# Kernel optimization log

Hardware: AMD Instinct MI355X
Metric: run time of the kernel (lower is better)

The kernel has to match this reference:

```python
import jax, jax.numpy as jnp
import numpy as np

B, T = 1024, 39
NUM_C, NUM_STU, NUM_E, EMB = 123, 100000, 50000, 256
H = 123
IN1 = NUM_C + EMB  # 379


def setup_inputs() -> dict:
    key = jax.random.key(0)
    ks = jax.random.split(key, 32)
    f = lambda k, shp, s: jax.random.normal(k, shp, dtype=jnp.float32) * s
    inp = {}
    inp["q_maritx"] = jax.random.uniform(ks[0], (B, T, NUM_C), dtype=jnp.float32)
    inp["q_maritx_next"] = jax.random.uniform(ks[1], (B, T, NUM_C), dtype=jnp.float32)
    inp["concept"] = jax.random.randint(ks[2], (B, T), 0, NUM_C + 1)
    inp["s_id"] = jax.random.randint(ks[3], (B, 1), 0, NUM_STU + 1)
    inp["e_id"] = jax.random.randint(ks[4], (B, T), 0, NUM_E + 1)
    inp["r"] = jax.random.randint(ks[5], (B, T), 0, 2)
    inp["q_next"] = jax.random.randint(ks[6], (B, T), 0, NUM_E + 1)
    inp["concept_next"] = jax.random.randint(ks[7], (B, T), 0, NUM_C + 1)
    # learned parameters
    inp["emb_problem"] = f(ks[8], (NUM_E + 1, EMB), 1.0)
    inp["student_W"] = f(ks[9], (NUM_STU + 1, NUM_C), 1.0)
    inp["k_diff_W"] = f(ks[10], (NUM_E + 1, NUM_C), 1.0)
    inp["e_disc_W"] = f(ks[11], (NUM_E + 1, 1), 1.0)
    inp["answer_W"] = f(ks[12], (2, EMB), 1.0)
    inp["zz_W"] = f(ks[13], (NUM_C, NUM_C), 0.05)
    inp["zz_b"] = jnp.zeros((NUM_C,), jnp.float32)
    inp["d_t"] = f(ks[14], (1,), 1.0)
    inp["d_e"] = f(ks[15], (1,), 1.0)
    inp["W_ih"] = f(ks[16], (H, IN1), 0.05)
    inp["b_ih"] = jnp.zeros((H,), jnp.float32)
    inp["W_hh"] = f(ks[17], (H, H), 0.05)
    inp["b_hh"] = jnp.zeros((H,), jnp.float32)
    inp["W_tg"] = f(ks[18], (H, 1), 0.05)
    inp["b_tg"] = jnp.zeros((H,), jnp.float32)
    inp["W_z"] = f(ks[19], (H, IN1 + H), 0.05)
    inp["b_z"] = jnp.zeros((H,), jnp.float32)
    inp["W_h"] = f(ks[20], (H, IN1 + H), 0.05)
    inp["b_h"] = jnp.zeros((H,), jnp.float32)
    inp["p1_W"] = f(ks[21], (256, 502), 0.05)
    inp["p1_b"] = jnp.zeros((256,), jnp.float32)
    inp["p2_W"] = f(ks[22], (123, 256), 0.05)
    inp["p2_b"] = jnp.zeros((123,), jnp.float32)
    inp["p3_W"] = f(ks[23], (1, 123), 0.05)
    inp["p3_b"] = jnp.zeros((1,), jnp.float32)
    return inp


def _forward(q_maritx, q_maritx_next, emb_problem, student_W, k_diff_W, e_disc_W,
             answer_W, zz_W, zz_b, d_t, d_e, W_ih, b_ih, W_hh, b_hh, W_tg, b_tg,
             W_z, b_z, W_h, b_h, p1_W, p1_b, p2_W, p2_b, p3_W, p3_b,
             s_id, e_id, r, q_next):
    Bc, Tc = e_id.shape
    e_next_emb = emb_problem[q_next]                       # [B,T,256]
    s_prof = jax.nn.sigmoid(student_W[s_id])               # [B,1,123] (broadcasts vs repeat(1,39,1))
    k_diff = jax.nn.sigmoid(k_diff_W[e_id])                # [B,T,123]
    e_disc = jax.nn.sigmoid(e_disc_W[e_id]) * d_e          # [B,T,1]
    r_emb = answer_W[r]                                    # [B,T,256]
    concept_ab = jnp.einsum('btk,hk->bth', q_maritx, zz_W) + zz_b  # [B,T,123]
    x1 = jnp.concatenate([concept_ab * s_prof, r_emb], axis=-1)    # [B,T,379]
    # --- time-gated RNN: h_t = tanh(W_ih x_t + W_hh h + b) * sigmoid(tg(t)) ---
    Xp = jnp.einsum('bti,hi->bth', x1, W_ih) + b_ih
    tvec = jnp.arange(Tc, dtype=Xp.dtype)[:, None]
    gates = jax.nn.sigmoid(tvec * W_tg[:, 0][None, :] + b_tg)      # [T,123]
    h0 = jnp.zeros((Bc, W_hh.shape[0]), Xp.dtype)

    def step1(h, xs):
        xp, g = xs
        h = jnp.tanh(xp + h @ W_hh.T + b_hh) * g
        return h, h

    _, ys1 = jax.lax.scan(step1, h0, (Xp.transpose(1, 0, 2), gates))
    out_zz = ys1.transpose(1, 0, 2)                        # [B,T,123]
    # --- GRU-like cell (W_r unused in original forward) ---
    input_x1 = e_disc * (d_t * s_prof + (1.0 - d_t) * out_zz - k_diff) * q_maritx
    x2 = jnp.concatenate([input_x1, r_emb], axis=-1)       # [B,T,379]
    nin = x2.shape[-1]
    Wz_x, Wz_h = W_z[:, :nin], W_z[:, nin:]
    Wh_x, Wh_h = W_h[:, :nin], W_h[:, nin:]
    Zx = jnp.einsum('bti,hi->bth', x2, Wz_x) + b_z
    Hx = jnp.einsum('bti,hi->bth', x2, Wh_x) + b_h

    def step2(h, xs):
        zx, hx = xs
        z = jax.nn.sigmoid(zx + h @ Wz_h.T)
        ht = jnp.tanh(hx + h @ Wh_h.T)
        h = (1.0 - z) * h + z * ht
        return h, h

    _, ys2 = jax.lax.scan(step2, h0, (Zx.transpose(1, 0, 2), Hx.transpose(1, 0, 2)))
    outputs = ys2.transpose(1, 0, 2)                       # [B,T,123]
    hcat = jnp.concatenate([outputs, e_next_emb, q_maritx_next], axis=-1)  # [B,T,502]
    o1 = jax.nn.sigmoid(hcat @ p1_W.T + p1_b)  # dropout as identity (deterministic reference)
    o2 = jax.nn.sigmoid(o1 @ p2_W.T + p2_b)
    return jax.nn.sigmoid(o2 @ p3_W.T + p3_b)              # [B,T,1]


def reference(q_maritx, q_maritx_next, emb_problem, student_W, k_diff_W, e_disc_W,
              answer_W, zz_W, zz_b, d_t, d_e, W_ih, b_ih, W_hh, b_hh, W_tg, b_tg,
              W_z, b_z, W_h, b_h, p1_W, p1_b, p2_W, p2_b, p3_W, p3_b,
              concept, s_id, e_id, r, q_next, concept_next):
    # concept / concept_next embeddings are computed but unused in the original output
    return _forward(q_maritx, q_maritx_next, emb_problem, student_W, k_diff_W,
                    e_disc_W, answer_W, zz_W, zz_b, d_t, d_e, W_ih, b_ih, W_hh,
                    b_hh, W_tg, b_tg, W_z, b_z, W_h, b_h, p1_W, p1_b, p2_W,
                    p2_b, p3_W, p3_b, s_id, e_id, r, q_next)
```

## Files before the change

### kernel.cpp

```cpp
#include <hip/hip_runtime.h>
#include <hip/hip_bf16.h>

#define NRB 39936
#define BB 1024
#define TT 39
#define CC 123
#define EMBD 256
#define PCH 136

typedef __attribute__((ext_vector_type(8))) short short8;
typedef __attribute__((ext_vector_type(4))) short shortv4;
typedef __attribute__((ext_vector_type(4))) float floatx4;
typedef unsigned short us;

__device__ __forceinline__ float rcp_(float x){ return __builtin_amdgcn_rcpf(x); }
__device__ __forceinline__ float fsig(float x){ return rcp_(1.f + __expf(-x)); }
__device__ __forceinline__ float ftanh(float x){
  float ax = __builtin_fabsf(x);
  float e = __expf(-2.f*ax);
  float r = (1.f - e) * rcp_(1.f + e);
  return __builtin_copysignf(r, x);
}
__device__ __forceinline__ us f2bf(float x){
  union { float f; unsigned u; } v; v.f = x;
  unsigned r = v.u + 0x7FFFu + ((v.u >> 16) & 1u);
  return (us)(r >> 16);
}
__device__ __forceinline__ us f2bfh(float x){
  __bf16 h = (__bf16)x;
  return __builtin_bit_cast(us, h);
}
__device__ __forceinline__ float bf2f(us u){
  union { unsigned u; float f; } v; v.u = ((unsigned)u) << 16; return v.f;
}

__device__ __forceinline__ void gl_lds16(void* lds, const void* g){
  __builtin_amdgcn_global_load_lds(
      (const __attribute__((address_space(1))) unsigned int*)g,
      (__attribute__((address_space(3))) unsigned int*)lds, 16, 0, 0);
}

#define G_RC 6
#define G_CW 1088
#define G_CAST 2496
#define G_HCAT 1872
#define G_PRE (G_RC + G_CW + G_CAST + G_HCAT)

__global__ __launch_bounds__(256) void k_pre(
    const float* __restrict__ W_ih, const float* __restrict__ W_z,
    const float* __restrict__ W_h, const float* __restrict__ answer_W,
    const float* __restrict__ zz_W, const float* __restrict__ W_hh,
    const float* __restrict__ p1_W, const float* __restrict__ p2_W,
    const float* __restrict__ emb, const int* __restrict__ q_next,
    const float* __restrict__ qmn, const float* __restrict__ q_m,
    float* __restrict__ rtab, us* __restrict__ wts,
    us* __restrict__ p1bf, us* __restrict__ p2bf,
    us* __restrict__ qbf, us* __restrict__ Abf)
{
  const int blk = blockIdx.x, tid = threadIdx.x;
  if (blk < G_RC){
    int which = blk >> 1, j = blk & 1, h = tid;
    if (h >= CC) return;
    const float* W; int stride;
    if (which==0){ W=W_ih; stride=379; } else if (which==1){ W=W_z; stride=502; } else { W=W_h; stride=502; }
    const float* a = answer_W + j*EMBD;
    const float* w = W + (size_t)h*stride + CC;
    float acc = 0.f;
    #pragma unroll 8
    for (int i=0;i<EMBD;i++) acc += w[i]*a[i];
    rtab[(which*2+j)*128 + h] = acc;
    return;
  }
  if (blk < G_RC + G_CW){
    int i = (blk - G_RC)*256 + tid;
    if (i < 7*16384){
      int w = i >> 14, idx = i & 16383, n = idx >> 7, k = idx & 127;
      float v = 0.f;
      if (n < CC && k < CC){
        if      (w==0) v = zz_W[n*CC + k];
        else if (w==1) v = W_ih[n*379 + k];
        else if (w==2) v = W_z [n*502 + k];
        else if (w==3) v = W_h [n*502 + k];
        else if (w==4) v = W_hh[n*CC + k];
        else if (w==5) v = W_z [n*502 + 379 + k];
        else           v = W_h [n*502 + 379 + k];
      }
      wts[i] = f2bf(v);
      return;
    }
    int j = i - 7*16384;
    if (j < 256*512){
      int n = j >> 9, k = j & 511;
      float v;
      if      (k < 379) v = p1_W[n*502 + k + 123];
      else if (k < 384) v = 0.f;
      else if (k < 507) v = p1_W[n*502 + (k - 384)];
      else              v = 0.f;
      p1bf[j] = f2bf(v);
      return;
    }
    j -= 256*512;
    if (j < 128*256){
      int n = j >> 8, k = j & 255;
      p2bf[j] = f2bf(n < CC ? p2_W[n*256 + k] : 0.f);
    }
    return;
  }
  if (blk < G_RC + G_CW + G_CAST){
    const size_t total = (size_t)NRB*128;
    for (size_t i = (size_t)(blk - G_RC - G_CW)*256 + tid; i < total; i += (size_t)G_CAST*256){
      int col = (int)(i & 127); size_t rp = i >> 7;
      int t = (int)(rp >> 10), b = (int)(rp & 1023);
      float v = (col < CC) ? q_m[((size_t)b*TT + t)*CC + col] : 0.f;
      qbf[i] = f2bf(v);
    }
    return;
  }
  {
    const size_t nchunk = (size_t)NRB*48;
    for (size_t c = (size_t)(blk - G_RC - G_CW - G_CAST)*256 + tid; c < nchunk; c += (size_t)G_HCAT*256){
      size_t row = c / 48;
      int c0 = (int)(c - row*48) * 8;
      short8 o;
      if (c0 < 256){
        int qn = q_next[row];
        float4 v0 = *(const float4*)(emb + (size_t)qn*EMBD + c0);
        float4 v1 = *(const float4*)(emb + (size_t)qn*EMBD + c0 + 4);
        o[0]=f2bf(v0.x); o[1]=f2bf(v0.y); o[2]=f2bf(v0.z); o[3]=f2bf(v0.w);
        o[4]=f2bf(v1.x); o[5]=f2bf(v1.y); o[6]=f2bf(v1.z); o[7]=f2bf(v1.w);
      } else {
        int j0 = c0 - 256;
        #pragma unroll
        for (int jj=0;jj<8;jj++){
          int j = j0 + jj;
          o[jj] = (j < CC) ? f2bf(qmn[row*CC + j]) : (short)0;
        }
      }
      *(short8*)(Abf + row*512 + c0) = o;
    }
  }
}

__global__ __launch_bounds__(256) void k_zz_elem(
    const us* __restrict__ X, const us* __restrict__ W,
    const float* __restrict__ zz_b,
    const float* __restrict__ q_m, const int* __restrict__ s_id,
    const int* __restrict__ e_id, const float* __restrict__ student_W,
    const float* __restrict__ k_diff_W, const float* __restrict__ e_disc_W,
    const float* __restrict__ d_t_p, const float* __restrict__ d_e_p,
    us* __restrict__ x1a, us* __restrict__ pre2, us* __restrict__ cqb)
{
  __shared__ __align__(16) us Asl[16][64][8];
  const int tid = threadIdx.x, w = tid >> 6, l = tid & 63, q = l >> 4, r16 = l & 15;
  const int rTile = blockIdx.x*64;
  short8 bfr[2][4];
  #pragma unroll
  for (int nt=0;nt<2;nt++){
    int n = w*32 + nt*16 + r16;
    #pragma unroll
    for (int kt=0;kt<4;kt++)
      bfr[nt][kt] = *(const short8*)(W + (size_t)n*128 + kt*32 + q*8);
  }
  #pragma unroll
  for (int i=0;i<4;i++){
    int seg = i*4 + w;
    gl_lds16(&Asl[seg][l][0], X + (size_t)(rTile+l)*128 + seg*8);
  }
  floatx4 acc[4][2];
  #pragma unroll
  for (int mt=0;mt<4;mt++){
    #pragma unroll
    for (int nt=0;nt<2;nt++){ acc[mt][nt][0]=0.f; acc[mt][nt][1]=0.f; acc[mt][nt][2]=0.f; acc[mt][nt][3]=0.f; }
  }
  __syncthreads();
  #pragma unroll
  for (int kt=0;kt<4;kt++){
    short8 af[4];
    #pragma unroll
    for (int mt=0;mt<4;mt++) af[mt] = *(const short8*)&Asl[kt*4+q][mt*16+r16][0];
    #pragma unroll
    for (int mt=0;mt<4;mt++){
      #pragma unroll
      for (int nt=0;nt<2;nt++)
        acc[mt][nt] = __builtin_amdgcn_mfma_f32_16x16x32_bf16(af[mt], bfr[nt][kt], acc[mt][nt], 0,0,0);
    }
  }
  const float dt = d_t_p[0], de = d_e_p[0];
  float zzb[2]; int colv[2];
  #pragma unroll
  for (int nt=0;nt<2;nt++){
    int col = w*32 + nt*16 + r16; colv[nt] = col;
    zzb[nt] = (col < CC) ? zz_b[col] : 0.f;
  }
  const int t = rTile >> 10;
  #pragma unroll
  for (int mt=0;mt<4;mt++){
    #pragma unroll
    for (int i=0;i<4;i++){
      int row = rTile + mt*16 + q*4 + i;
      int b = row & 1023;
      int g = b*TT + t;
      int btile = b >> 4, r = b & 15;
      int sid = s_id[b];
      int e   = e_id[g];
      float ed = fsig(e_disc_W[e]) * de;
      size_t base = ((size_t)t*64 + btile)*2048;
      #pragma unroll
      for (int nt=0;nt<2;nt++){
        int col = colv[nt];
        float x1v = 0.f, p2v = 0.f, cqv = 0.f;
        if (col < CC){
          float ab = acc[mt][nt][i] + zzb[nt];
          float sp = fsig(student_W[(size_t)sid*CC + col]);
          float kd = fsig(k_diff_W[(size_t)e*CC + col]);
          float qv = q_m[(size_t)g*CC + col];
          x1v = ab*sp;
          p2v = ed*(dt*sp - kd)*qv;
          cqv = ed*(1.f - dt)*qv;
        }
        x1a[base + (size_t)(((col>>5)*64 + ((col>>3)&3)*16 + r)*8) + (col&7)] = f2bf(x1v);
        size_t off = base + (size_t)(((col>>5)*64 + ((r>>2))*16 + (col&15))*8) + ((col>>4)&1)*4 + (r&3);
        pre2[off] = f2bf(p2v);
        cqb[off]  = f2bf(cqv);
      }
    }
  }
}

__global__ __launch_bounds__(512,1) void k_mid(
    const us* __restrict__ x1a, const us* __restrict__ pre2, const us* __restrict__ cqb,
    const us* __restrict__ Wih, const us* __restrict__ Whh,
    const us* __restrict__ Wzx, const us* __restrict__ Whx,
    const us* __restrict__ Wzh, const us* __restrict__ Whh2,
    const float* __restrict__ b_ih, const float* __restrict__ b_z, const float* __restrict__ b_h,
    const float* __restrict__ W_tg, const float* __restrict__ b_tg,
    const float* __restrict__ rtab, const int* __restrict__ r_idx,
    us* __restrict__ Abf)
{
  __shared__ __align__(16) us h1s[2][16*PCH];
  __shared__ __align__(16) us x2s[2][16*PCH];
  __shared__ __align__(16) us h2s[2][16*PCH];
  __shared__ int rint[TT*16];
  __shared__ __align__(16) us lds_pad[27680];

  const int tid = threadIdx.x, wid = tid >> 6, l = tid & 63, q = l >> 4, r16 = l & 15;
  const bool isA = wid < 4;
  const int gw = wid & 3;
  const int bbase = blockIdx.x*16;
  const int n0 = gw*32 + r16, n1 = n0 + 16;
  if (Abf == (us*)0) lds_pad[tid] = (us)tid;

  short8 w[4][2][4];
  if (isA){
    #pragma unroll
    for (int tt=0;tt<2;tt++){
      const int nn = n0 + tt*16;
      #pragma unroll
      for (int kt=0;kt<4;kt++){
        size_t wofs = (size_t)nn*128 + kt*32 + q*8;
        w[0][tt][kt] = *(const short8*)(Wih + wofs);
        w[1][tt][kt] = *(const short8*)(Whh + wofs);
      }
    }
  } else {
    #pragma unroll
    for (int tt=0;tt<2;tt++){
      const int nn = n0 + tt*16;
      #pragma unroll
      for (int kt=0;kt<4;kt++){
        size_t wofs = (size_t)nn*128 + kt*32 + q*8;
        w[0][tt][kt] = *(const short8*)(Wzx + wofs);
        w[1][tt][kt] = *(const short8*)(Wzh + wofs);
        w[2][tt][kt] = *(const short8*)(Whx + wofs);
        w[3][tt][kt] = *(const short8*)(Whh2 + wofs);
      }
    }
  }

  const bool v0 = n0 < CC, v1 = n1 < CC;
  float ia0[2], ia1[2], ib0[2], ib1[2];
  float wg0=0.f, bg0=0.f, wg1=0.f, bg1=0.f;
  if (isA){
    ia0[0] = v0 ? b_ih[n0] + rtab[n0]     : 0.f;
    ia1[0] = v0 ? b_ih[n0] + rtab[128+n0] : 0.f;
    ia0[1] = v1 ? b_ih[n1] + rtab[n1]     : 0.f;
    ia1[1] = v1 ? b_ih[n1] + rtab[128+n1] : 0.f;
    ib0[0]=0.f; ib1[0]=0.f; ib0[1]=0.f; ib1[1]=0.f;
    wg0 = v0 ? W_tg[n0]:0.f; bg0 = v0 ? b_tg[n0]:0.f;
    wg1 = v1 ? W_tg[n1]:0.f; bg1 = v1 ? b_tg[n1]:0.f;
  } else {
    ia0[0] = v0 ? b_z[n0] + rtab[256+n0] : 0.f;
    ia1[0] = v0 ? b_z[n0] + rtab[384+n0] : 0.f;
    ia0[1] = v1 ? b_z[n1] + rtab[256+n1] : 0.f;
    ia1[1] = v1 ? b_z[n1] + rtab[384+n1] : 0.f;
    ib0[0] = v0 ? b_h[n0] + rtab[512+n0] : 0.f;
    ib1[0] = v0 ? b_h[n0] + rtab[640+n0] : 0.f;
    ib0[1] = v1 ? b_h[n1] + rtab[512+n1] : 0.f;
    ib1[1] = v1 ? b_h[n1] + rtab[640+n1] : 0.f;
  }

  for (int i = tid; i < TT*16; i += 512)
    rint[i] = r_idx[(size_t)(bbase + (i & 15))*TT + (i >> 4)];
  for (int i = tid; i < 16*PCH; i += 512){ h1s[1][i] = 0; h2s[1][i] = 0; }

  short8 x1c[4]; short8 pc8, cc8;
  if (isA){
    size_t base = (size_t)blockIdx.x*2048;
    #pragma unroll
    for (int kt=0;kt<4;kt++)
      x1c[kt] = *(const short8*)(x1a + base + (size_t)(kt*64 + q*16 + r16)*8);
    size_t cofs = base + (size_t)(gw*64 + q*16 + r16)*8;
    pc8 = *(const short8*)(pre2 + cofs);
    cc8 = *(const short8*)(cqb + cofs);
  }
  __syncthreads();

  floatx4 accx0, accx1;
  if (isA){
    int4 rs = *(const int4*)&rint[q*4];
    accx0[0] = rs.x ? ia1[0] : ia0[0];  accx1[0] = rs.x ? ia1[1] : ia0[1];
    accx0[1] = rs.y ? ia1[0] : ia0[0];  accx1[1] = rs.y ? ia1[1] : ia0[1];
    accx0[2] = rs.z ? ia1[0] : ia0[0];  accx1[2] = rs.z ? ia1[1] : ia0[1];
    accx0[3] = rs.w ? ia1[0] : ia0[0];  accx1[3] = rs.w ? ia1[1] : ia0[1];
    #pragma unroll
    for (int kt=0;kt<4;kt++){
      accx0 = __builtin_amdgcn_mfma_f32_16x16x32_bf16(x1c[kt], w[0][0][kt], accx0, 0,0,0);
      accx1 = __builtin_amdgcn_mfma_f32_16x16x32_bf16(x1c[kt], w[0][1][kt], accx1, 0,0,0);
    }
  }
  floatx4 hold0, hold1;
  hold0[0]=0.f; hold0[1]=0.f; hold0[2]=0.f; hold0[3]=0.f;
  hold1[0]=0.f; hold1[1]=0.f; hold1[2]=0.f; hold1[3]=0.f;

  for (int k=0; k<=TT; ++k){
    const int pA = k & 1;
    if (isA){
      short8 x1n[4]; short8 pcn, ccn;
      if (k+1 < TT){
        size_t base = ((size_t)(k+1)*64 + blockIdx.x)*2048;
        #pragma unroll
        for (int kt=0;kt<4;kt++)
          x1n[kt] = *(const short8*)(x1a + base + (size_t)(kt*64 + q*16 + r16)*8);
        size_t cofs = base + (size_t)(gw*64 + q*16 + r16)*8;
        pcn = *(const short8*)(pre2 + cofs);
        ccn = *(const short8*)(cqb + cofs);
      }
      if (k < TT){
        short8 fr1[4];
        #pragma unroll
        for (int kt=0;kt<4;kt++)
          fr1[kt] = *(const short8*)&h1s[pA^1][r16*PCH + kt*32 + q*8];
        floatx4 a0 = accx0, a1 = accx1;
        #pragma unroll
        for (int kt=0;kt<4;kt++){
          a0 = __builtin_amdgcn_mfma_f32_16x16x32_bf16(fr1[kt], w[1][0][kt], a0, 0,0,0);
          a1 = __builtin_amdgcn_mfma_f32_16x16x32_bf16(fr1[kt], w[1][1][kt], a1, 0,0,0);
        }
        float g0 = fsig((float)k*wg0 + bg0);
        float g1 = fsig((float)k*wg1 + bg1);
        #pragma unroll
        for (int i=0;i<4;i++){
          float h1v0 = ftanh(a0[i]) * g0;
          h1s[pA][(q*4+i)*PCH + n0] = f2bfh(h1v0);
          float xv0 = bf2f((us)pc8[i]) + bf2f((us)cc8[i])*h1v0;
          x2s[pA][(q*4+i)*PCH + n0] = f2bfh(xv0);
          float h1v1 = ftanh(a1[i]) * g1;
          h1s[pA][(q*4+i)*PCH + n1] = f2bfh(h1v1);
          float xv1 = bf2f((us)pc8[4+i]) + bf2f((us)cc8[4+i])*h1v1;
          x2s[pA][(q*4+i)*PCH + n1] = f2bfh(xv1);
        }
      }
      if (k >= 2){
        int row = tid >> 4, cs = tid & 15;
        short8 hv8 = *(const short8*)&h2s[pA][row*PCH + cs*8];
        *(short8*)(Abf + ((size_t)(bbase + row)*TT + (k-2))*512 + 384 + cs*8) = hv8;
      }
      if (k+1 < TT){
        int4 rs = *(const int4*)&rint[(k+1)*16 + q*4];
        accx0[0] = rs.x ? ia1[0] : ia0[0];  accx1[0] = rs.x ? ia1[1] : ia0[1];
        accx0[1] = rs.y ? ia1[0] : ia0[0];  accx1[1] = rs.y ? ia1[1] : ia0[1];
        accx0[2] = rs.z ? ia1[0] : ia0[0];  accx1[2] = rs.z ? ia1[1] : ia0[1];
        accx0[3] = rs.w ? ia1[0] : ia0[0];  accx1[3] = rs.w ? ia1[1] : ia0[1];
        #pragma unroll
        for (int kt=0;kt<4;kt++){
          accx0 = __builtin_amdgcn_mfma_f32_16x16x32_bf16(x1n[kt], w[0][0][kt], accx0, 0,0,0);
          accx1 = __builtin_amdgcn_mfma_f32_16x16x32_bf16(x1n[kt], w[0][1][kt], accx1, 0,0,0);
        }
        pc8 = pcn; cc8 = ccn;
      }
    } else if (k >= 1){
      const int t = k-1, pB = t & 1;
      short8 fx[4], fh[4];
      #pragma unroll
      for (int kt=0;kt<4;kt++){
        fx[kt] = *(const short8*)&x2s[pB][r16*PCH + kt*32 + q*8];
        fh[kt] = *(const short8*)&h2s[pB^1][r16*PCH + kt*32 + q*8];
      }
      int4 rs = *(const int4*)&rint[t*16 + q*4];
      floatx4 az0, az1, ah0, ah1;
      az0[0] = rs.x ? ia1[0] : ia0[0];  ah0[0] = rs.x ? ib1[0] : ib0[0];
      az0[1] = rs.y ? ia1[0] : ia0[0];  ah0[1] = rs.y ? ib1[0] : ib0[0];
      az0[2] = rs.z ? ia1[0] : ia0[0];  ah0[2] = rs.z ? ib1[0] : ib0[0];
      az0[3] = rs.w ? ia1[0] : ia0[0];  ah0[3] = rs.w ? ib1[0] : ib0[0];
      az1[0] = rs.x ? ia1[1] : ia0[1];  ah1[0] = rs.x ? ib1[1] : ib0[1];
      az1[1] = rs.y ? ia1[1] : ia0[1];  ah1[1] = rs.y ? ib1[1] : ib0[1];
      az1[2] = rs.z ? ia1[1] : ia0[1];  ah1[2] = rs.z ? ib1[1] : ib0[1];
      az1[3] = rs.w ? ia1[1] : ia0[1];  ah1[3] = rs.w ? ib1[1] : ib0[1];
      #pragma unroll
      for (int kt=0;kt<4;kt++){
        az0 = __builtin_amdgcn_mfma_f32_16x16x32_bf16(fx[kt], w[0][0][kt], az0, 0,0,0);
        az0 = __builtin_amdgcn_mfma_f32_16x16x32_bf16(fh[kt], w[1][0][kt], az0, 0,0,0);
        ah0 = __builtin_amdgcn_mfma_f32_16x16x32_bf16(fx[kt], w[2][0][kt], ah0, 0,0,0);
        ah0 = __builtin_amdgcn_mfma_f32_16x16x32_bf16(fh[kt], w[3][0][kt], ah0, 0,0,0);
        az1 = __builtin_amdgcn_mfma_f32_16x16x32_bf16(fx[kt], w[0][1][kt], az1, 0,0,0);
        az1 = __builtin_amdgcn_mfma_f32_16x16x32_bf16(fh[kt], w[1][1][kt], az1, 0,0,0);
        ah1 = __builtin_amdgcn_mfma_f32_16x16x32_bf16(fx[kt], w[2][1][kt], ah1, 0,0,0);
        ah1 = __builtin_amdgcn_mfma_f32_16x16x32_bf16(fh[kt], w[3][1][kt], ah1, 0,0,0);
      }
      #pragma unroll
      for (int i=0;i<4;i++){
        float z0  = fsig(az0[i]);
        float th0 = ftanh(ah0[i]);
        hold0[i] += z0*(th0 - hold0[i]);
        h2s[pB][(q*4+i)*PCH + n0] = f2bfh(hold0[i]);
        float z1  = fsig(az1[i]);
        float th1 = ftanh(ah1[i]);
        hold1[i] += z1*(th1 - hold1[i]);
        h2s[pB][(q*4+i)*PCH + n1] = f2bfh(hold1[i]);
      }
    }
    __syncthreads();
  }
  if (tid < 256){
    int row = tid >> 4, cs = tid & 15;
    short8 hv8 = *(const short8*)&h2s[(TT-1)&1][row*PCH + cs*8];
    *(short8*)(Abf + ((size_t)(bbase + row)*TT + (TT-1))*512 + 384 + cs*8) = hv8;
  }
}

__global__ __launch_bounds__(256) void k_out(
    const us* __restrict__ Abf, const us* __restrict__ p1bf,
    const float* __restrict__ p1_b, const us* __restrict__ p2bf,
    const float* __restrict__ p2_b, const float* __restrict__ p3_W,
    const float* __restrict__ p3_b, float* __restrict__ out)
{
  __shared__ __align__(16) us smem[20480];
  __shared__ float red[64][4];
  us* Asl = smem;
  us* Bsl = smem + 4096;
  us* o1s = smem;
  const int tid = threadIdx.x;
  const int w = tid >> 6, l = tid & 63;
  const int q = l >> 4, r16 = l & 15;
  const int rTile = blockIdx.x * 64;
  floatx4 acc[4][4];
  #pragma unroll
  for (int a=0;a<4;a++){
    #pragma unroll
    for (int b=0;b<4;b++){ acc[a][b][0]=0.f; acc[a][b][1]=0.f; acc[a][b][2]=0.f; acc[a][b][3]=0.f; }
  }
  for (int c = 0; c < 8; c++){
    const int k0 = c*64;
    #pragma unroll
    for (int i=0;i<2;i++){
      int u = i*256 + tid; int seg = u>>6, m = u&63;
      gl_lds16(&Asl[(seg*64 + m)*8], Abf + (size_t)(rTile+m)*512 + k0 + seg*8);
    }
    #pragma unroll
    for (int i=0;i<8;i++){
      int u = i*256 + tid; int seg = u>>8, nn = u&255;
      gl_lds16(&Bsl[(seg*256 + nn)*8], p1bf + (size_t)nn*512 + k0 + seg*8);
    }
    __syncthreads();
    #pragma unroll
    for (int ks=0; ks<2; ks++){
      int seg = ks*4 + q;
      short8 af[4], bfr[4];
      #pragma unroll
      for (int mt=0;mt<4;mt++) af[mt] = *(const short8*)&Asl[(seg*64 + mt*16 + r16)*8];
      #pragma unroll
      for (int nt=0;nt<4;nt++) bfr[nt] = *(const short8*)&Bsl[(seg*256 + w*64 + nt*16 + r16)*8];
      #pragma unroll
      for (int mt=0;mt<4;mt++){
        #pragma unroll
        for (int nt=0;nt<4;nt++)
          acc[mt][nt] = __builtin_amdgcn_mfma_f32_16x16x32_bf16(af[mt], bfr[nt], acc[mt][nt], 0,0,0);
      }
    }
    __syncthreads();
  }
  #pragma unroll
  for (int nt=0;nt<4;nt++){
    int col = w*64 + nt*16 + r16;
    float bb = p1_b[col];
    #pragma unroll
    for (int mt=0;mt<4;mt++){
      #pragma unroll
      for (int i=0;i<4;i++)
        o1s[(mt*16 + q*4 + i)*264 + col] = f2bf(fsig(acc[mt][nt][i] + bb));
    }
  }
  __syncthreads();
  short8 bf2[2][8];
  #pragma unroll
  for (int nt=0;nt<2;nt++){
    int n2 = w*32 + nt*16 + r16;
    #pragma unroll
    for (int kt=0;kt<8;kt++)
      bf2[nt][kt] = *(const short8*)(p2bf + (size_t)n2*256 + kt*32 + q*8);
  }
  floatx4 ac2[4][2];
  #pragma unroll
  for (int mt=0;mt<4;mt++){
    #pragma unroll
    for (int nt=0;nt<2;nt++){ ac2[mt][nt][0]=0.f; ac2[mt][nt][1]=0.f; ac2[mt][nt][2]=0.f; ac2[mt][nt][3]=0.f; }
  }
  #pragma unroll
  for (int kt=0;kt<8;kt++){
    short8 af[4];
    #pragma unroll
    for (int mt=0;mt<4;mt++) af[mt] = *(const short8*)&o1s[(mt*16 + r16)*264 + kt*32 + q*8];
    #pragma unroll
    for (int mt=0;mt<4;mt++){
      #pragma unroll
      for (int nt=0;nt<2;nt++)
        ac2[mt][nt] = __builtin_amdgcn_mfma_f32_16x16x32_bf16(af[mt], bf2[nt][kt], ac2[mt][nt], 0,0,0);
    }
  }
  const int n0 = w*32 + r16, n1 = n0 + 16;
  const float pb0 = (n0<CC)? p2_b[n0]:0.f, pb1 = (n1<CC)? p2_b[n1]:0.f;
  const float p30 = (n0<CC)? p3_W[n0]:0.f, p31 = (n1<CC)? p3_W[n1]:0.f;
  #pragma unroll
  for (int mt=0;mt<4;mt++){
    #pragma unroll
    for (int i=0;i<4;i++){
      float s = fsig(ac2[mt][0][i]+pb0)*p30 + fsig(ac2[mt][1][i]+pb1)*p31;
      s += __shfl_xor(s,1,16); s += __shfl_xor(s,2,16);
      s += __shfl_xor(s,4,16); s += __shfl_xor(s,8,16);
      if (r16==0) red[mt*16 + q*4 + i][w] = s;
    }
  }
  __syncthreads();
  if (tid < 64){
    float o = red[tid][0]+red[tid][1]+red[tid][2]+red[tid][3] + p3_b[0];
    out[rTile + tid] = fsig(o);
  }
}

extern "C" void kernel_launch(void* const* d_in, const int* in_sizes, int n_in,
                              void* d_out, int out_size, void* d_ws, size_t ws_size,
                              hipStream_t stream) {
  const float* q_m       = (const float*)d_in[0];
  const float* q_m_next  = (const float*)d_in[1];
  const int*   s_id      = (const int*)d_in[3];
  const int*   e_id      = (const int*)d_in[4];
  const int*   r_idx     = (const int*)d_in[5];
  const int*   q_next    = (const int*)d_in[6];
  const float* emb_problem = (const float*)d_in[8];
  const float* student_W = (const float*)d_in[9];
  const float* k_diff_W  = (const float*)d_in[10];
  const float* e_disc_W  = (const float*)d_in[11];
  const float* answer_W  = (const float*)d_in[12];
  const float* zz_W      = (const float*)d_in[13];
  const float* zz_b      = (const float*)d_in[14];
  const float* d_t       = (const float*)d_in[15];
  const float* d_e       = (const float*)d_in[16];
  const float* W_ih      = (const float*)d_in[17];
  const float* b_ih      = (const float*)d_in[18];
  const float* W_hh      = (const float*)d_in[19];
  const float* W_tg      = (const float*)d_in[21];
  const float* b_tg      = (const float*)d_in[22];
  const float* W_z       = (const float*)d_in[23];
  const float* b_z       = (const float*)d_in[24];
  const float* W_h       = (const float*)d_in[25];
  const float* b_h       = (const float*)d_in[26];
  const float* p1_W      = (const float*)d_in[27];
  const float* p1_b      = (const float*)d_in[28];
  const float* p2_W      = (const float*)d_in[29];
  const float* p2_b      = (const float*)d_in[30];
  const float* p3_W      = (const float*)d_in[31];
  const float* p3_b      = (const float*)d_in[32];

  float* ws   = (float*)d_ws;
  float* rtab = ws;
  us* qbf  = (us*)(ws + 1024);
  us* x1a  = qbf  + (size_t)NRB*128;
  us* pre2 = x1a  + (size_t)NRB*128;
  us* cqb  = pre2 + (size_t)NRB*128;
  us* Abf  = cqb  + (size_t)NRB*128;
  us* wts  = Abf  + (size_t)NRB*512;
  us* p1bf = wts  + 7*16384;
  us* p2bf = p1bf + 256*512;

  const us* zzWbf  = wts + 0*16384;
  const us* Wih123 = wts + 1*16384;
  const us* Wz123  = wts + 2*16384;
  const us* Wh123  = wts + 3*16384;
  const us* Whhbf  = wts + 4*16384;
  const us* Wzhbf  = wts + 5*16384;
  const us* Whh2bf = wts + 6*16384;

  hipLaunchKernelGGL(k_pre, dim3(G_PRE), dim3(256), 0, stream,
                     W_ih, W_z, W_h, answer_W, zz_W, W_hh, p1_W, p2_W,
                     emb_problem, q_next, q_m_next, q_m,
                     rtab, wts, p1bf, p2bf, qbf, Abf);
  hipLaunchKernelGGL(k_zz_elem, dim3(NRB/64), dim3(256), 0, stream,
                     qbf, zzWbf, zz_b, q_m, s_id, e_id, student_W, k_diff_W,
                     e_disc_W, d_t, d_e, x1a, pre2, cqb);
  hipLaunchKernelGGL(k_mid, dim3(BB/16), dim3(512), 0, stream,
                     x1a, pre2, cqb, Wih123, Whhbf, Wz123, Wh123, Wzhbf, Whh2bf,
                     b_ih, b_z, b_h, W_tg, b_tg, rtab, r_idx, Abf);
  hipLaunchKernelGGL(k_out, dim3(NRB/64), dim3(256), 0, stream,
                     Abf, p1bf, p1_b, p2bf, p2_b, p3_W, p3_b, (float*)d_out);
}
```

Before: 370.9 us.

## Hoist input projection of first RNN out of recurrence into batched kernel

```diff
diff --git a/kernel.cpp b/kernel.cpp
--- a/kernel.cpp
+++ b/kernel.cpp
@@ -227,9 +227,56 @@
   }
 }
 
+__global__ __launch_bounds__(256) void k_xp(
+    us* __restrict__ x1a, us* __restrict__ qbf, const us* __restrict__ Wih)
+{
+  const int tid = threadIdx.x, w = tid >> 6, l = tid & 63, q = l >> 4, r16 = l & 15;
+  const int rTile = blockIdx.x*64;
+  const int tbase = rTile >> 4;
+  short8 bfr[2][4];
+  #pragma unroll
+  for (int nt=0;nt<2;nt++){
+    int n = w*32 + nt*16 + r16;
+    #pragma unroll
+    for (int kt=0;kt<4;kt++)
+      bfr[nt][kt] = *(const short8*)(Wih + (size_t)n*128 + kt*32 + q*8);
+  }
+  floatx4 acc[4][2];
+  #pragma unroll
+  for (int mt=0;mt<4;mt++){
+    #pragma unroll
+    for (int nt=0;nt<2;nt++){ acc[mt][nt][0]=0.f; acc[mt][nt][1]=0.f; acc[mt][nt][2]=0.f; acc[mt][nt][3]=0.f; }
+  }
+  #pragma unroll
+  for (int kt=0;kt<4;kt++){
+    short8 af[4];
+    #pragma unroll
+    for (int mt=0;mt<4;mt++)
+      af[mt] = *(const short8*)(x1a + (size_t)(tbase+mt)*2048 + (size_t)(kt*64 + q*16 + r16)*8);
+    #pragma unroll
+    for (int mt=0;mt<4;mt++){
+      #pragma unroll
+      for (int nt=0;nt<2;nt++)
+        acc[mt][nt] = __builtin_amdgcn_mfma_f32_16x16x32_bf16(af[mt], bfr[nt][kt], acc[mt][nt], 0,0,0);
+    }
+  }
+  __syncthreads();
+  #pragma unroll
+  for (int mt=0;mt<4;mt++){
+    #pragma unroll
+    for (int nt=0;nt<2;nt++){
+      int col = w*32 + nt*16 + r16;
+      float* fb = (col < 64) ? (float*)(x1a + (size_t)(tbase+mt)*2048)
+                             : (float*)(qbf + (size_t)(tbase+mt)*2048);
+      *(floatx4*)(fb + (size_t)(col & 63)*16 + q*4) = acc[mt][nt];
+    }
+  }
+}
+
 __global__ __launch_bounds__(512,1) void k_mid(
-    const us* __restrict__ x1a, const us* __restrict__ pre2, const us* __restrict__ cqb,
-    const us* __restrict__ Wih, const us* __restrict__ Whh,
+    const us* __restrict__ xpa, const us* __restrict__ xpb,
+    const us* __restrict__ pre2, const us* __restrict__ cqb,
+    const us* __restrict__ Whh,
     const us* __restrict__ Wzx, const us* __restrict__ Whx,
     const us* __restrict__ Wzh, const us* __restrict__ Whh2,
     const float* __restrict__ b_ih, const float* __restrict__ b_z, const float* __restrict__ b_h,
@@ -241,14 +288,14 @@
   __shared__ __align__(16) us x2s[2][16*PCH];
   __shared__ __align__(16) us h2s[2][16*PCH];
   __shared__ int rint[TT*16];
-  __shared__ __align__(16) us lds_pad[27680];
 
   const int tid = threadIdx.x, wid = tid >> 6, l = tid & 63, q = l >> 4, r16 = l & 15;
   const bool isA = wid < 4;
   const int gw = wid & 3;
   const int bbase = blockIdx.x*16;
   const int n0 = gw*32 + r16, n1 = n0 + 16;
-  if (Abf == (us*)0) lds_pad[tid] = (us)tid;
+  const int e7 = r16 & 7;
+  const int cb0 = (gw<<2) | (r16>>3);
 
   short8 w[4][2][4];
   if (isA){
@@ -256,11 +303,8 @@
     for (int tt=0;tt<2;tt++){
       const int nn = n0 + tt*16;
       #pragma unroll
-      for (int kt=0;kt<4;kt++){
-        size_t wofs = (size_t)nn*128 + kt*32 + q*8;
-        w[0][tt][kt] = *(const short8*)(Wih + wofs);
-        w[1][tt][kt] = *(const short8*)(Whh + wofs);
-      }
+      for (int kt=0;kt<4;kt++)
+        w[0][tt][kt] = *(const short8*)(Whh + (size_t)nn*128 + kt*32 + q*8);
     }
   } else {
     #pragma unroll
@@ -303,31 +347,20 @@
     rint[i] = r_idx[(size_t)(bbase + (i & 15))*TT + (i >> 4)];
   for (int i = tid; i < 16*PCH; i += 512){ h1s[1][i] = 0; h2s[1][i] = 0; }
 
-  short8 x1c[4]; short8 pc8, cc8;
+  const float* xpbase = (gw < 2) ? (const float*)xpa : (const float*)xpb;
+  const int xoff = (((gw&1)*32 + r16)*16 + q*4);
+
+  float4 xc0, xc1; short8 pc8, cc8;
   if (isA){
-    size_t base = (size_t)blockIdx.x*2048;
-    #pragma unroll
-    for (int kt=0;kt<4;kt++)
-      x1c[kt] = *(const short8*)(x1a + base + (size_t)(kt*64 + q*16 + r16)*8);
-    size_t cofs = base + (size_t)(gw*64 + q*16 + r16)*8;
+    const float* fb = xpbase + (size_t)blockIdx.x*1024 + xoff;
+    xc0 = *(const float4*)fb;
+    xc1 = *(const float4*)(fb + 256);
+    size_t cofs = (size_t)blockIdx.x*2048 + (size_t)(gw*64 + q*16 + r16)*8;
     pc8 = *(const short8*)(pre2 + cofs);
     cc8 = *(const short8*)(cqb + cofs);
   }
   __syncthreads();
 
-  floatx4 accx0, accx1;
-  if (isA){
-    int4 rs = *(const int4*)&rint[q*4];
-    accx0[0] = rs.x ? ia1[0] : ia0[0];  accx1[0] = rs.x ? ia1[1] : ia0[1];
-    accx0[1] = rs.y ? ia1[0] : ia0[0];  accx1[1] = rs.y ? ia1[1] : ia0[1];
-    accx0[2] = rs.z ? ia1[0] : ia0[0];  accx1[2] = rs.z ? ia1[1] : ia0[1];
-    accx0[3] = rs.w ? ia1[0] : ia0[0];  accx1[3] = rs.w ? ia1[1] : ia0[1];
-    #pragma unroll
-    for (int kt=0;kt<4;kt++){
-      accx0 = __builtin_amdgcn_mfma_f32_16x16x32_bf16(x1c[kt], w[0][0][kt], accx0, 0,0,0);
-      accx1 = __builtin_amdgcn_mfma_f32_16x16x32_bf16(x1c[kt], w[0][1][kt], accx1, 0,0,0);
-    }
-  }
   floatx4 hold0, hold1;
   hold0[0]=0.f; hold0[1]=0.f; hold0[2]=0.f; hold0[3]=0.f;
   hold1[0]=0.f; hold1[1]=0.f; hold1[2]=0.f; hold1[3]=0.f;
@@ -335,13 +368,13 @@
   for (int k=0; k<=TT; ++k){
     const int pA = k & 1;
     if (isA){
-      short8 x1n[4]; short8 pcn, ccn;
+      float4 xn0, xn1; short8 pcn, ccn;
       if (k+1 < TT){
-        size_t base = ((size_t)(k+1)*64 + blockIdx.x)*2048;
-        #pragma unroll
-        for (int kt=0;kt<4;kt++)
-          x1n[kt] = *(const short8*)(x1a + base + (size_t)(kt*64 + q*16 + r16)*8);
-        size_t cofs = base + (size_t)(gw*64 + q*16 + r16)*8;
+        size_t tnext = (size_t)(k+1)*64 + blockIdx.x;
+        const float* fb = xpbase + tnext*1024 + xoff;
+        xn0 = *(const float4*)fb;
+        xn1 = *(const float4*)(fb + 256);
+        size_t cofs = tnext*2048 + (size_t)(gw*64 + q*16 + r16)*8;
         pcn = *(const short8*)(pre2 + cofs);
         ccn = *(const short8*)(cqb + cofs);
       }
@@ -349,52 +382,47 @@
         short8 fr1[4];
         #pragma unroll
         for (int kt=0;kt<4;kt++)
-          fr1[kt] = *(const short8*)&h1s[pA^1][r16*PCH + kt*32 + q*8];
-        floatx4 a0 = accx0, a1 = accx1;
+          fr1[kt] = *(const short8*)&h1s[pA^1][r16*PCH + ((kt*4+q)^e7)*8];
+        int4 rs = *(const int4*)&rint[k*16 + q*4];
+        floatx4 a0, a1;
+        a0[0] = (rs.x ? ia1[0] : ia0[0]) + xc0.x;  a1[0] = (rs.x ? ia1[1] : ia0[1]) + xc1.x;
+        a0[1] = (rs.y ? ia1[0] : ia0[0]) + xc0.y;  a1[1] = (rs.y ? ia1[1] : ia0[1]) + xc1.y;
+        a0[2] = (rs.z ? ia1[0] : ia0[0]) + xc0.z;  a1[2] = (rs.z ? ia1[1] : ia0[1]) + xc1.z;
+        a0[3] = (rs.w ? ia1[0] : ia0[0]) + xc0.w;  a1[3] = (rs.w ? ia1[1] : ia0[1]) + xc1.w;
         #pragma unroll
         for (int kt=0;kt<4;kt++){
-          a0 = __builtin_amdgcn_mfma_f32_16x16x32_bf16(fr1[kt], w[1][0][kt], a0, 0,0,0);
-          a1 = __builtin_amdgcn_mfma_f32_16x16x32_bf16(fr1[kt], w[1][1][kt], a1, 0,0,0);
+          a0 = __builtin_amdgcn_mfma_f32_16x16x32_bf16(fr1[kt], w[0][0][kt], a0, 0,0,0);
+          a1 = __builtin_amdgcn_mfma_f32_16x16x32_bf16(fr1[kt], w[0][1][kt], a1, 0,0,0);
         }
         float g0 = fsig((float)k*wg0 + bg0);
         float g1 = fsig((float)k*wg1 + bg1);
         #pragma unroll
         for (int i=0;i<4;i++){
+          int row = q*4+i;
+          int sb0 = row*PCH + ((cb0      ^ (row&7))*8) + e7;
+          int sb1 = row*PCH + (((cb0+2)  ^ (row&7))*8) + e7;
           float h1v0 = ftanh(a0[i]) * g0;
-          h1s[pA][(q*4+i)*PCH + n0] = f2bfh(h1v0);
-          float xv0 = bf2f((us)pc8[i]) + bf2f((us)cc8[i])*h1v0;
-          x2s[pA][(q*4+i)*PCH + n0] = f2bfh(xv0);
+          h1s[pA][sb0] = f2bfh(h1v0);
+          x2s[pA][sb0] = f2bfh(bf2f((us)pc8[i]) + bf2f((us)cc8[i])*h1v0);
           float h1v1 = ftanh(a1[i]) * g1;
-          h1s[pA][(q*4+i)*PCH + n1] = f2bfh(h1v1);
-          float xv1 = bf2f((us)pc8[4+i]) + bf2f((us)cc8[4+i])*h1v1;
-          x2s[pA][(q*4+i)*PCH + n1] = f2bfh(xv1);
+          h1s[pA][sb1] = f2bfh(h1v1);
+          x2s[pA][sb1] = f2bfh(bf2f((us)pc8[4+i]) + bf2f((us)cc8[4+i])*h1v1);
         }
       }
       if (k >= 2){
         int row = tid >> 4, cs = tid & 15;
-        short8 hv8 = *(const short8*)&h2s[pA][row*PCH + cs*8];
+        short8 hv8 = *(const short8*)&h2s[pA][row*PCH + ((cs ^ (row&7))*8)];
         *(short8*)(Abf + ((size_t)(bbase + row)*TT + (k-2))*512 + 384 + cs*8) = hv8;
       }
-      if (k+1 < TT){
-        int4 rs = *(const int4*)&rint[(k+1)*16 + q*4];
-        accx0[0] = rs.x ? ia1[0] : ia0[0];  accx1[0] = rs.x ? ia1[1] : ia0[1];
-        accx0[1] = rs.y ? ia1[0] : ia0[0];  accx1[1] = rs.y ? ia1[1] : ia0[1];
-        accx0[2] = rs.z ? ia1[0] : ia0[0];  accx1[2] = rs.z ? ia1[1] : ia0[1];
-        accx0[3] = rs.w ? ia1[0] : ia0[0];  accx1[3] = rs.w ? ia1[1] : ia0[1];
-        #pragma unroll
-        for (int kt=0;kt<4;kt++){
-          accx0 = __builtin_amdgcn_mfma_f32_16x16x32_bf16(x1n[kt], w[0][0][kt], accx0, 0,0,0);
-          accx1 = __builtin_amdgcn_mfma_f32_16x16x32_bf16(x1n[kt], w[0][1][kt], accx1, 0,0,0);
-        }
-        pc8 = pcn; cc8 = ccn;
-      }
+      if (k+1 < TT){ xc0 = xn0; xc1 = xn1; pc8 = pcn; cc8 = ccn; }
     } else if (k >= 1){
       const int t = k-1, pB = t & 1;
       short8 fx[4], fh[4];
       #pragma unroll
       for (int kt=0;kt<4;kt++){
-        fx[kt] = *(const short8*)&x2s[pB][r16*PCH + kt*32 + q*8];
-        fh[kt] = *(const short8*)&h2s[pB^1][r16*PCH + kt*32 + q*8];
+        int sidx = r16*PCH + ((kt*4+q)^e7)*8;
+        fx[kt] = *(const short8*)&x2s[pB][sidx];
+        fh[kt] = *(const short8*)&h2s[pB^1][sidx];
       }
       int4 rs = *(const int4*)&rint[t*16 + q*4];
       floatx4 az0, az1, ah0, ah1;
@@ -419,21 +447,24 @@
       }
       #pragma unroll
       for (int i=0;i<4;i++){
+        int row = q*4+i;
+        int sb0 = row*PCH + ((cb0     ^ (row&7))*8) + e7;
+        int sb1 = row*PCH + (((cb0+2) ^ (row&7))*8) + e7;
         float z0  = fsig(az0[i]);
         float th0 = ftanh(ah0[i]);
         hold0[i] += z0*(th0 - hold0[i]);
-        h2s[pB][(q*4+i)*PCH + n0] = f2bfh(hold0[i]);
+        h2s[pB][sb0] = f2bfh(hold0[i]);
         float z1  = fsig(az1[i]);
         float th1 = ftanh(ah1[i]);
         hold1[i] += z1*(th1 - hold1[i]);
-        h2s[pB][(q*4+i)*PCH + n1] = f2bfh(hold1[i]);
+        h2s[pB][sb1] = f2bfh(hold1[i]);
       }
     }
     __syncthreads();
   }
   if (tid < 256){
     int row = tid >> 4, cs = tid & 15;
-    short8 hv8 = *(const short8*)&h2s[(TT-1)&1][row*PCH + cs*8];
+    short8 hv8 = *(const short8*)&h2s[(TT-1)&1][row*PCH + ((cs ^ (row&7))*8)];
     *(short8*)(Abf + ((size_t)(bbase + row)*TT + (TT-1))*512 + 384 + cs*8) = hv8;
   }
 }
@@ -607,8 +638,10 @@
   hipLaunchKernelGGL(k_zz_elem, dim3(NRB/64), dim3(256), 0, stream,
                      qbf, zzWbf, zz_b, q_m, s_id, e_id, student_W, k_diff_W,
                      e_disc_W, d_t, d_e, x1a, pre2, cqb);
+  hipLaunchKernelGGL(k_xp, dim3(NRB/64), dim3(256), 0, stream,
+                     x1a, qbf, Wih123);
   hipLaunchKernelGGL(k_mid, dim3(BB/16), dim3(512), 0, stream,
-                     x1a, pre2, cqb, Wih123, Whhbf, Wz123, Wh123, Wzhbf, Whh2bf,
+                     x1a, qbf, pre2, cqb, Whhbf, Wz123, Wh123, Wzhbf, Whh2bf,
                      b_ih, b_z, b_h, W_tg, b_tg, rtab, r_idx, Abf);
   hipLaunchKernelGGL(k_out, dim3(NRB/64), dim3(256), 0, stream,
                      Abf, p1bf, p1_b, p2bf, p2_b, p3_W, p3_b, (float*)d_out);
```

Result: slower. 383.0 us (+3.2%).

## Fuse q_m bf16 cast into zz GEMM and move hcat gather into zz kernel

Applied to the files above, without the earlier changes.

```diff
diff --git a/kernel.cpp b/kernel.cpp
--- a/kernel.cpp
+++ b/kernel.cpp
@@ -42,20 +42,17 @@
 
 #define G_RC 6
 #define G_CW 1088
-#define G_CAST 2496
-#define G_HCAT 1872
-#define G_PRE (G_RC + G_CW + G_CAST + G_HCAT)
+#define G_PRE (G_RC + G_CW)
+#define G_ZZ (NRB/64)
+#define G_HC 1248
 
 __global__ __launch_bounds__(256) void k_pre(
     const float* __restrict__ W_ih, const float* __restrict__ W_z,
     const float* __restrict__ W_h, const float* __restrict__ answer_W,
     const float* __restrict__ zz_W, const float* __restrict__ W_hh,
     const float* __restrict__ p1_W, const float* __restrict__ p2_W,
-    const float* __restrict__ emb, const int* __restrict__ q_next,
-    const float* __restrict__ qmn, const float* __restrict__ q_m,
     float* __restrict__ rtab, us* __restrict__ wts,
-    us* __restrict__ p1bf, us* __restrict__ p2bf,
-    us* __restrict__ qbf, us* __restrict__ Abf)
+    us* __restrict__ p1bf, us* __restrict__ p2bf)
 {
   const int blk = blockIdx.x, tid = threadIdx.x;
   if (blk < G_RC){
@@ -71,7 +68,7 @@
     rtab[(which*2+j)*128 + h] = acc;
     return;
   }
-  if (blk < G_RC + G_CW){
+  {
     int i = (blk - G_RC)*256 + tid;
     if (i < 7*16384){
       int w = i >> 14, idx = i & 16383, n = idx >> 7, k = idx & 127;
@@ -104,21 +101,26 @@
       int n = j >> 8, k = j & 255;
       p2bf[j] = f2bf(n < CC ? p2_W[n*256 + k] : 0.f);
     }
-    return;
-  }
-  if (blk < G_RC + G_CW + G_CAST){
-    const size_t total = (size_t)NRB*128;
-    for (size_t i = (size_t)(blk - G_RC - G_CW)*256 + tid; i < total; i += (size_t)G_CAST*256){
-      int col = (int)(i & 127); size_t rp = i >> 7;
-      int t = (int)(rp >> 10), b = (int)(rp & 1023);
-      float v = (col < CC) ? q_m[((size_t)b*TT + t)*CC + col] : 0.f;
-      qbf[i] = f2bf(v);
-    }
-    return;
-  }
-  {
+  }
+}
+
+__global__ __launch_bounds__(256) void k_zz_elem(
+    const us* __restrict__ W,
+    const float* __restrict__ zz_b,
+    const float* __restrict__ q_m, const int* __restrict__ s_id,
+    const int* __restrict__ e_id, const float* __restrict__ student_W,
+    const float* __restrict__ k_diff_W, const float* __restrict__ e_disc_W,
+    const float* __restrict__ d_t_p, const float* __restrict__ d_e_p,
+    us* __restrict__ x1a, us* __restrict__ pre2, us* __restrict__ cqb,
+    const float* __restrict__ emb, const int* __restrict__ q_next,
+    const float* __restrict__ qmn, us* __restrict__ Abf)
+{
+  __shared__ __align__(16) us Asl[16][64][8];
+  const int tid = threadIdx.x;
+
+  if (blockIdx.x >= G_ZZ){
     const size_t nchunk = (size_t)NRB*48;
-    for (size_t c = (size_t)(blk - G_RC - G_CW - G_CAST)*256 + tid; c < nchunk; c += (size_t)G_HCAT*256){
+    for (size_t c = (size_t)(blockIdx.x - G_ZZ)*256 + tid; c < nchunk; c += (size_t)G_HC*256){
       size_t row = c / 48;
       int c0 = (int)(c - row*48) * 8;
       short8 o;
@@ -138,21 +140,12 @@
       }
       *(short8*)(Abf + row*512 + c0) = o;
     }
-  }
-}
-
-__global__ __launch_bounds__(256) void k_zz_elem(
-    const us* __restrict__ X, const us* __restrict__ W,
-    const float* __restrict__ zz_b,
-    const float* __restrict__ q_m, const int* __restrict__ s_id,
-    const int* __restrict__ e_id, const float* __restrict__ student_W,
-    const float* __restrict__ k_diff_W, const float* __restrict__ e_disc_W,
-    const float* __restrict__ d_t_p, const float* __restrict__ d_e_p,
-    us* __restrict__ x1a, us* __restrict__ pre2, us* __restrict__ cqb)
-{
-  __shared__ __align__(16) us Asl[16][64][8];
-  const int tid = threadIdx.x, w = tid >> 6, l = tid & 63, q = l >> 4, r16 = l & 15;
+    return;
+  }
+
+  const int w = tid >> 6, l = tid & 63, q = l >> 4, r16 = l & 15;
   const int rTile = blockIdx.x*64;
+  const int t = rTile >> 10;
   short8 bfr[2][4];
   #pragma unroll
   for (int nt=0;nt<2;nt++){
@@ -161,10 +154,22 @@
     for (int kt=0;kt<4;kt++)
       bfr[nt][kt] = *(const short8*)(W + (size_t)n*128 + kt*32 + q*8);
   }
-  #pragma unroll
-  for (int i=0;i<4;i++){
-    int seg = i*4 + w;
-    gl_lds16(&Asl[seg][l][0], X + (size_t)(rTile+l)*128 + seg*8);
+  {
+    const int seg = tid & 15;
+    const int rr  = tid >> 4;
+    #pragma unroll
+    for (int p = 0; p < 4; ++p){
+      int row = p*16 + rr;
+      int b = (rTile + row) & 1023;
+      const float* qrow = q_m + ((size_t)b*TT + t)*CC + seg*8;
+      short8 o;
+      #pragma unroll
+      for (int j=0;j<8;j++){
+        int col = seg*8 + j;
+        o[j] = (col < CC) ? f2bf(qrow[j]) : (short)0;
+      }
+      *(short8*)&Asl[seg][row][0] = o;
+    }
   }
   floatx4 acc[4][2];
   #pragma unroll
@@ -192,7 +197,6 @@
     int col = w*32 + nt*16 + r16; colv[nt] = col;
     zzb[nt] = (col < CC) ? zz_b[col] : 0.f;
   }
-  const int t = rTile >> 10;
   #pragma unroll
   for (int mt=0;mt<4;mt++){
     #pragma unroll
@@ -241,14 +245,12 @@
   __shared__ __align__(16) us x2s[2][16*PCH];
   __shared__ __align__(16) us h2s[2][16*PCH];
   __shared__ int rint[TT*16];
-  __shared__ __align__(16) us lds_pad[27680];
 
   const int tid = threadIdx.x, wid = tid >> 6, l = tid & 63, q = l >> 4, r16 = l & 15;
   const bool isA = wid < 4;
   const int gw = wid & 3;
   const int bbase = blockIdx.x*16;
   const int n0 = gw*32 + r16, n1 = n0 + 16;
-  if (Abf == (us*)0) lds_pad[tid] = (us)tid;
 
   short8 w[4][2][4];
   if (isA){
@@ -602,11 +604,11 @@
 
   hipLaunchKernelGGL(k_pre, dim3(G_PRE), dim3(256), 0, stream,
                      W_ih, W_z, W_h, answer_W, zz_W, W_hh, p1_W, p2_W,
-                     emb_problem, q_next, q_m_next, q_m,
-                     rtab, wts, p1bf, p2bf, qbf, Abf);
-  hipLaunchKernelGGL(k_zz_elem, dim3(NRB/64), dim3(256), 0, stream,
-                     qbf, zzWbf, zz_b, q_m, s_id, e_id, student_W, k_diff_W,
-                     e_disc_W, d_t, d_e, x1a, pre2, cqb);
+                     rtab, wts, p1bf, p2bf);
+  hipLaunchKernelGGL(k_zz_elem, dim3(G_ZZ + G_HC), dim3(256), 0, stream,
+                     zzWbf, zz_b, q_m, s_id, e_id, student_W, k_diff_W,
+                     e_disc_W, d_t, d_e, x1a, pre2, cqb,
+                     emb_problem, q_next, q_m_next, Abf);
   hipLaunchKernelGGL(k_mid, dim3(BB/16), dim3(512), 0, stream,
                      x1a, pre2, cqb, Wih123, Whhbf, Wz123, Wh123, Wzhbf, Whh2bf,
                      b_ih, b_z, b_h, W_tg, b_tg, rtab, r_idx, Abf);
```

Result: slower. 390.6 us (+5.3%).
